# Optimization experiments

Measured on AMD Instinct MI355X. Metric: run time of the kernel, lower is better.

The kernel has to match this reference:

```python
import jax, jax.numpy as jnp
import numpy as np
from jax import lax

EPS = 1e-4


def setup_inputs() -> dict:
    key = jax.random.key(0)
    k1, k2, k3, k4, k5 = jax.random.split(key, 5)
    B, F, P, C = 8192, 512, 64, 100
    return {
        "x": jax.random.normal(k1, (B, F), dtype=jnp.float32),
        "w": jax.random.normal(k2, (P, F), dtype=jnp.float32),
        "xi": jax.random.normal(k3, (1, P), dtype=jnp.float32),
        "eta": jax.random.normal(k4, (1, P), dtype=jnp.float32),
        "beta": jax.random.normal(k5, (P, C), dtype=jnp.float32),
    }


def reference(x, w, xi, eta, beta):
    # Distance layer: squared Euclidean distance to each prototype -> [B, P]
    # ||w_p - x||^2 expressed as GEMM form (same math, efficient)
    d = (jnp.sum(x * x, axis=-1, keepdims=True)
         - 2.0 * (x @ w.T)
         + jnp.sum(w * w, axis=-1))  # [B, P]

    # Distance activation: si = sigmoid(xi) * exp(-eta^2 * d), scaled by per-sample max
    gamma = eta * eta                       # [1, P]
    alpha = jax.nn.sigmoid(xi)              # [1, P]
    si = jnp.exp(-gamma * d) * alpha        # [B, P]
    si = si / (jnp.max(si, axis=-1, keepdims=True) + EPS)

    # Belief masses: u_p normalized beta^2 rows -> mass [B, P, C]
    beta_sq = beta * beta
    u = beta_sq / jnp.sum(beta_sq, axis=-1, keepdims=True)  # [P, C]
    mass = si[..., None] * u[None]                           # [B, P, C]

    # Omega: append residual uncertainty channel -> [B, P, C+1]
    omega = 1.0 - jnp.sum(mass, axis=-1, keepdims=True)
    mass_omega = jnp.concatenate([mass, omega], axis=-1)

    # Sequential Dempster combination over prototypes
    masses = jnp.moveaxis(mass_omega, 1, 0)  # [P, B, C+1]

    def step(m1, m2):
        omega1 = m1[..., -1:]
        omega2 = m2[..., -1:]
        c = m1 * m2 + m1 * omega2 + omega1 * m2
        c = c / (jnp.sum(c, axis=-1, keepdims=True) + EPS)
        return c, None

    m_final, _ = lax.scan(step, masses[0], masses[1:])  # [B, C+1]

    # Final normalization
    return m_final / jnp.sum(m_final, axis=-1, keepdims=True)
```

## Files before the change

### kernel.cpp

```cpp
#include <hip/hip_runtime.h>
#include <math.h>

#define NB 8192
#define NF 512
#define NP 64
#define NC 100
#define NR 16
#define EPSF 1e-4f
#define LOG2E 1.44269504088896340736f

using short8  = __attribute__((ext_vector_type(8))) short;
using floatx4 = __attribute__((ext_vector_type(4))) float;

__device__ __forceinline__ short2 bsplit(float v) {
  unsigned b = __float_as_uint(v);
  short h = (short)(b >> 16);
  float hf = __uint_as_float(b & 0xFFFF0000u);
  float lo = v - hf;
  short l = (short)(__float_as_uint(lo) >> 16);
  return make_short2(h, l);
}

__global__ __launch_bounds__(256, 2)
void ds_fused2(const float* __restrict__ x, const float* __restrict__ w,
               const float* __restrict__ xi, const float* __restrict__ eta,
               const float* __restrict__ beta, float* __restrict__ out)
{
  __shared__ __align__(16) short xhi_l[NR * 136];
  __shared__ __align__(16) short xlo_l[NR * 136];
  __shared__ __align__(16) char  wu_l[64 * 136 * 2 * 2];
  __shared__ __align__(16) float d_l[NR * 68];
  __shared__ __align__(16) float si_l[NR * 64];
  __shared__ float sqp_l[NR * 17];
  __shared__ float red_l[256];
  __shared__ float xsql[NR];
  __shared__ float wsql[64], alph_l[64], kgam_l[64], binv_l[64];
  short* whi_l = (short*)wu_l;
  short* wlo_l = (short*)(wu_l + 64 * 136 * 2);
  float* u_l   = (float*)wu_l;

  const int t  = threadIdx.x;
  const int R0 = blockIdx.x * NR;

  const int xr_row = t >> 4, xr_sl = t & 15;
  const int wr_p   = t >> 2, wr_q  = t & 3;
  const int wv = t >> 6;
  const int ml = t & 15;
  const int qd = (t & 63) >> 4;

  float xsq_acc = 0.f, wsq_acc = 0.f;
  floatx4 acc0 = {0.f, 0.f, 0.f, 0.f};
  floatx4 acc1 = {0.f, 0.f, 0.f, 0.f};

  for (int ch = 0; ch < 4; ++ch) {
    const int kb = ch * 128;
    __syncthreads();
    {
      const float* xr = x + (size_t)(R0 + xr_row) * NF + kb + xr_sl * 8;
      float4 a = *(const float4*)&xr[0];
      float4 b = *(const float4*)&xr[4];
      xsq_acc += a.x*a.x + a.y*a.y + a.z*a.z + a.w*a.w
               + b.x*b.x + b.y*b.y + b.z*b.z + b.w*b.w;
      short8 hv, lv;
      short2 s0 = bsplit(a.x), s1 = bsplit(a.y), s2 = bsplit(a.z), s3 = bsplit(a.w);
      short2 s4 = bsplit(b.x), s5 = bsplit(b.y), s6 = bsplit(b.z), s7 = bsplit(b.w);
      hv[0]=s0.x; hv[1]=s1.x; hv[2]=s2.x; hv[3]=s3.x;
      hv[4]=s4.x; hv[5]=s5.x; hv[6]=s6.x; hv[7]=s7.x;
      lv[0]=s0.y; lv[1]=s1.y; lv[2]=s2.y; lv[3]=s3.y;
      lv[4]=s4.y; lv[5]=s5.y; lv[6]=s6.y; lv[7]=s7.y;
      *(short8*)&xhi_l[xr_row * 136 + xr_sl * 8] = hv;
      *(short8*)&xlo_l[xr_row * 136 + xr_sl * 8] = lv;
    }
    {
      const float* wr = w + (size_t)wr_p * NF + kb + wr_q * 32;
      #pragma unroll
      for (int g = 0; g < 4; ++g) {
        float4 a = *(const float4*)&wr[g * 8];
        float4 b = *(const float4*)&wr[g * 8 + 4];
        wsq_acc += a.x*a.x + a.y*a.y + a.z*a.z + a.w*a.w
                 + b.x*b.x + b.y*b.y + b.z*b.z + b.w*b.w;
        short8 hv, lv;
        short2 s0 = bsplit(a.x), s1 = bsplit(a.y), s2 = bsplit(a.z), s3 = bsplit(a.w);
        short2 s4 = bsplit(b.x), s5 = bsplit(b.y), s6 = bsplit(b.z), s7 = bsplit(b.w);
        hv[0]=s0.x; hv[1]=s1.x; hv[2]=s2.x; hv[3]=s3.x;
        hv[4]=s4.x; hv[5]=s5.x; hv[6]=s6.x; hv[7]=s7.x;
        lv[0]=s0.y; lv[1]=s1.y; lv[2]=s2.y; lv[3]=s3.y;
        lv[4]=s4.y; lv[5]=s5.y; lv[6]=s6.y; lv[7]=s7.y;
        *(short8*)&whi_l[wr_p * 136 + wr_q * 32 + g * 8] = hv;
        *(short8*)&wlo_l[wr_p * 136 + wr_q * 32 + g * 8] = lv;
      }
    }
    __syncthreads();
    #pragma unroll
    for (int ks = 0; ks < 4; ++ks) {
      short8 ah = *(const short8*)&xhi_l[ml * 136 + ks * 32 + qd * 8];
      short8 al = *(const short8*)&xlo_l[ml * 136 + ks * 32 + qd * 8];
      short8 bh = *(const short8*)&whi_l[(wv * 16 + ml) * 136 + ks * 32 + qd * 8];
      short8 bl = *(const short8*)&wlo_l[(wv * 16 + ml) * 136 + ks * 32 + qd * 8];
      acc0 = __builtin_amdgcn_mfma_f32_16x16x32_bf16(ah, bh, acc0, 0, 0, 0);
      acc1 = __builtin_amdgcn_mfma_f32_16x16x32_bf16(ah, bl, acc1, 0, 0, 0);
      acc1 = __builtin_amdgcn_mfma_f32_16x16x32_bf16(al, bh, acc1, 0, 0, 0);
    }
  }

  {
    #pragma unroll
    for (int i = 0; i < 4; ++i) {
      const int row = qd * 4 + i;
      d_l[row * 68 + wv * 16 + ml] = acc0[i] + acc1[i];
    }
    sqp_l[xr_row * 17 + xr_sl] = xsq_acc;
    red_l[wr_q * 64 + wr_p]    = wsq_acc;
  }
  __syncthreads();
  if (t < NR) {
    float s = 0.f;
    #pragma unroll
    for (int q = 0; q < 16; ++q) s += sqp_l[t * 17 + q];
    xsql[t] = s;
  }
  if (t < 64) {
    wsql[t] = ((red_l[t] + red_l[64 + t]) + red_l[128 + t]) + red_l[192 + t];
    float e = eta[t];
    kgam_l[t] = -LOG2E * e * e;
    alph_l[t] = 1.f / (1.f + __expf(-xi[t]));
  }
  __syncthreads();

  {
    const int p4 = t >> 2, q4 = t & 3;
    const float* br = beta + p4 * NC + q4 * 25;
    float s = 0.f;
    #pragma unroll 5
    for (int j = 0; j < 25; ++j) { float b = br[j]; s = fmaf(b, b, s); }
    red_l[q4 * 64 + p4] = s;
  }
  {
    const int row = t >> 4, p = (t & 15) * 4;
    float4 dt = *(const float4*)&d_l[row * 68 + p];
    const float xs = xsql[row];
    float si0 = alph_l[p+0] * exp2f(kgam_l[p+0] * (xs + wsql[p+0] - 2.f * dt.x));
    float si1 = alph_l[p+1] * exp2f(kgam_l[p+1] * (xs + wsql[p+1] - 2.f * dt.y));
    float si2 = alph_l[p+2] * exp2f(kgam_l[p+2] * (xs + wsql[p+2] - 2.f * dt.z));
    float si3 = alph_l[p+3] * exp2f(kgam_l[p+3] * (xs + wsql[p+3] - 2.f * dt.w));
    float mx = fmaxf(fmaxf(si0, si1), fmaxf(si2, si3));
    #pragma unroll
    for (int msk = 1; msk < 16; msk <<= 1) mx = fmaxf(mx, __shfl_xor(mx, msk, 64));
    const float rinv = 1.f / (mx + EPSF);
    float4 sv = make_float4(si0 * rinv, si1 * rinv, si2 * rinv, si3 * rinv);
    *(float4*)&si_l[row * 64 + p] = sv;
  }
  __syncthreads();
  if (t < 64) binv_l[t] = 1.f / (((red_l[t] + red_l[64 + t]) + red_l[128 + t]) + red_l[192 + t]);
  __syncthreads();
  {
    const int p4 = t >> 2, q4 = t & 3;
    const float bi = binv_l[p4];
    #pragma unroll
    for (int i = 0; i < 8; ++i) {
      const int q = q4 + 4 * i;
      float4 uv = make_float4(0.f, 0.f, 0.f, 0.f);
      if (q < 25) {
        const float* br = beta + p4 * NC + q * 4;
        float b0 = br[0], b1 = br[1], b2 = br[2], b3 = br[3];
        uv = make_float4(b0*b0*bi, b1*b1*bi, b2*b2*bi, b3*b3*bi);
      }
      *(float4*)&u_l[p4 * 128 + q * 4] = uv;
    }
  }
  __syncthreads();

  const int lane = t & 31;
  const bool isom = (lane == 25);
  #pragma unroll
  for (int pass = 0; pass < 2; ++pass) {
    const int row = pass * 8 + (t >> 5);
    const float* sirow = &si_l[row * 64];
    float4 u0 = *(const float4*)&u_l[lane * 4];
    float sp  = sirow[0];
    float m0 = sp * u0.x, m1 = sp * u0.y, m2 = sp * u0.z, m3 = sp * u0.w;
    float om1 = 1.f - sp;
    if (isom) m0 = om1;

    for (int p = 1; p < NP; ++p) {
      sp = sirow[p];
      float4 u = *(const float4*)&u_l[p * 128 + lane * 4];
      float om2 = 1.f - sp;
      float nom = -(om1 * om2);
      float t20 = fmaf(sp, u.x, om2);
      t20 = isom ? (om2 + om2) : t20;
      float t21 = fmaf(sp, u.y, om2);
      float t22 = fmaf(sp, u.z, om2);
      float t23 = fmaf(sp, u.w, om2);
      m0 = fmaf(m0 + om1, t20, nom);
      m1 = fmaf(m1 + om1, t21, nom);
      m2 = fmaf(m2 + om1, t22, nom);
      m3 = fmaf(m3 + om1, t23, nom);
      om1 = fmaf(nom, -2.f, -nom);
      if (isom) m0 = om1;
      if ((p & 3) == 0) {
        float ss = (m0 + m1) + (m2 + m3);
        #pragma unroll
        for (int msk = 1; msk < 32; msk <<= 1) ss += __shfl_xor(ss, msk, 64);
        float rn = __builtin_amdgcn_rcpf(ss);
        m0 *= rn; m1 *= rn; m2 *= rn; m3 *= rn; om1 *= rn;
      }
    }

    float ss = (m0 + m1) + (m2 + m3);
    #pragma unroll
    for (int msk = 1; msk < 32; msk <<= 1) ss += __shfl_xor(ss, msk, 64);
    float rn = 1.f / ss;
    m0 *= rn; m1 *= rn; m2 *= rn; m3 *= rn;

    float* orow = &out[(size_t)(R0 + row) * 101];
    if (lane < 25) {
      orow[lane*4+0] = m0; orow[lane*4+1] = m1;
      orow[lane*4+2] = m2; orow[lane*4+3] = m3;
    } else if (lane == 25) {
      orow[100] = m0;
    }
  }
}

extern "C" void kernel_launch(void* const* d_in, const int* in_sizes, int n_in,
                              void* d_out, int out_size, void* d_ws, size_t ws_size,
                              hipStream_t stream)
{
  const float* x    = (const float*)d_in[0];
  const float* w    = (const float*)d_in[1];
  const float* xi   = (const float*)d_in[2];
  const float* eta  = (const float*)d_in[3];
  const float* beta = (const float*)d_in[4];
  (void)d_ws; (void)ws_size;
  hipLaunchKernelGGL(ds_fused2, dim3(NB / NR), dim3(256), 0, stream,
                     x, w, xi, eta, beta, (float*)d_out);
}
```

Measured before the change: 95.66 us.

## Replace sequential Dempster scan with closed-form product recurrence and single-pass bf16 GEMM

The x·wᵀ GEMM drops the hi/lo bf16 split and runs as one truncated-bf16 MFMA pass with smaller K chunks. The per-row reductions now use shuffles instead of shared-memory partial sums, and the si computation reads directly from the MFMA accumulators. The 63-step sequential Dempster combination is rewritten as a closed-form product/scan: per-prototype scale factors come from a prefix product via shuffles, then a reverse loop accumulates a product and a weighted sum. Occupancy is raised to three blocks per CU. The aim is to cut the serial dependency chain and the GEMM cost, at the risk of precision loss from single bf16 truncation and of underflow or overflow from the powers of 3 and long products.

Result: faster. 85.17 us (-11.0%).

```diff
diff --git a/kernel.cpp b/kernel.cpp
--- a/kernel.cpp
+++ b/kernel.cpp
@@ -7,125 +7,91 @@
 #define NC 100
 #define NR 16
 #define EPSF 1e-4f
-#define LOG2E 1.44269504088896340736f
+#define LOG2E  1.44269504088896340736f
+#define LOG2_3 1.58496250072115618145f
 
 using short8  = __attribute__((ext_vector_type(8))) short;
 using floatx4 = __attribute__((ext_vector_type(4))) float;
 
-__device__ __forceinline__ short2 bsplit(float v) {
-  unsigned b = __float_as_uint(v);
-  short h = (short)(b >> 16);
-  float hf = __uint_as_float(b & 0xFFFF0000u);
-  float lo = v - hf;
-  short l = (short)(__float_as_uint(lo) >> 16);
-  return make_short2(h, l);
+__device__ __forceinline__ uint2 pkbf(float4 v) {
+  uint2 r;
+  r.x = (__float_as_uint(v.y) & 0xffff0000u) | (__float_as_uint(v.x) >> 16);
+  r.y = (__float_as_uint(v.w) & 0xffff0000u) | (__float_as_uint(v.z) >> 16);
+  return r;
 }
 
-__global__ __launch_bounds__(256, 2)
-void ds_fused2(const float* __restrict__ x, const float* __restrict__ w,
-               const float* __restrict__ xi, const float* __restrict__ eta,
-               const float* __restrict__ beta, float* __restrict__ out)
+#define OFF_XH    0
+#define OFF_WH    2304
+#define OFF_U     0
+#define OFF_PK4   32768
+#define OFF_SI    40960
+#define OFF_REDB  45056
+#define OFF_RMAX  46080
+#define OFF_UMAX  46336
+#define OFF_XSQL  46592
+#define OFF_WSQL  46656
+#define OFF_KGAM  46912
+#define OFF_ALPH  47168
+#define OFF_BINV  47424
+#define OFF_OMF   47680
+#define SMEM_SZ   47712
+
+__global__ __launch_bounds__(256, 3)
+void ds_one(const float* __restrict__ x, const float* __restrict__ w,
+            const float* __restrict__ xi, const float* __restrict__ eta,
+            const float* __restrict__ beta, float* __restrict__ out)
 {
-  __shared__ __align__(16) short xhi_l[NR * 136];
-  __shared__ __align__(16) short xlo_l[NR * 136];
-  __shared__ __align__(16) char  wu_l[64 * 136 * 2 * 2];
-  __shared__ __align__(16) float d_l[NR * 68];
-  __shared__ __align__(16) float si_l[NR * 64];
-  __shared__ float sqp_l[NR * 17];
-  __shared__ float red_l[256];
-  __shared__ float xsql[NR];
-  __shared__ float wsql[64], alph_l[64], kgam_l[64], binv_l[64];
-  short* whi_l = (short*)wu_l;
-  short* wlo_l = (short*)(wu_l + 64 * 136 * 2);
-  float* u_l   = (float*)wu_l;
-
-  const int t  = threadIdx.x;
-  const int R0 = blockIdx.x * NR;
-
-  const int xr_row = t >> 4, xr_sl = t & 15;
-  const int wr_p   = t >> 2, wr_q  = t & 3;
-  const int wv = t >> 6;
-  const int ml = t & 15;
-  const int qd = (t & 63) >> 4;
-
-  float xsq_acc = 0.f, wsq_acc = 0.f;
-  floatx4 acc0 = {0.f, 0.f, 0.f, 0.f};
-  floatx4 acc1 = {0.f, 0.f, 0.f, 0.f};
-
-  for (int ch = 0; ch < 4; ++ch) {
-    const int kb = ch * 128;
+  __shared__ __align__(16) char smem[SMEM_SZ];
+  short*  xh    = (short*)(smem + OFF_XH);
+  short*  wh    = (short*)(smem + OFF_WH);
+  float*  u_l   = (float*)(smem + OFF_U);
+  float4* pk4   = (float4*)(smem + OFF_PK4);
+  float*  si_l  = (float*)(smem + OFF_SI);
+  float*  redb  = (float*)(smem + OFF_REDB);
+  float*  rmax  = (float*)(smem + OFF_RMAX);
+  float*  umax  = (float*)(smem + OFF_UMAX);
+  float*  xsql  = (float*)(smem + OFF_XSQL);
+  float*  wsql  = (float*)(smem + OFF_WSQL);
+  float*  kgaml = (float*)(smem + OFF_KGAM);
+  float*  alphl = (float*)(smem + OFF_ALPH);
+  float*  binv  = (float*)(smem + OFF_BINV);
+  float*  omf   = (float*)(smem + OFF_OMF);
+
+  const int t    = threadIdx.x;
+  const int R0   = blockIdx.x * NR;
+  const int wv   = t >> 6;
+  const int ml   = t & 15;
+  const int qd   = (t & 63) >> 4;
+  const int xrow = t >> 4, xq = t & 15;
+  const int wl   = t & 63;
+
+  float xsq_acc = 0.f;
+  float wacc[4] = {0.f, 0.f, 0.f, 0.f};
+  floatx4 acc = {0.f, 0.f, 0.f, 0.f};
+
+  for (int ch = 0; ch < 8; ++ch) {
+    const int kb = ch * 64;
     __syncthreads();
     {
-      const float* xr = x + (size_t)(R0 + xr_row) * NF + kb + xr_sl * 8;
-      float4 a = *(const float4*)&xr[0];
-      float4 b = *(const float4*)&xr[4];
-      xsq_acc += a.x*a.x + a.y*a.y + a.z*a.z + a.w*a.w
-               + b.x*b.x + b.y*b.y + b.z*b.z + b.w*b.w;
-      short8 hv, lv;
-      short2 s0 = bsplit(a.x), s1 = bsplit(a.y), s2 = bsplit(a.z), s3 = bsplit(a.w);
-      short2 s4 = bsplit(b.x), s5 = bsplit(b.y), s6 = bsplit(b.z), s7 = bsplit(b.w);
-      hv[0]=s0.x; hv[1]=s1.x; hv[2]=s2.x; hv[3]=s3.x;
-      hv[4]=s4.x; hv[5]=s5.x; hv[6]=s6.x; hv[7]=s7.x;
-      lv[0]=s0.y; lv[1]=s1.y; lv[2]=s2.y; lv[3]=s3.y;
-      lv[4]=s4.y; lv[5]=s5.y; lv[6]=s6.y; lv[7]=s7.y;
-      *(short8*)&xhi_l[xr_row * 136 + xr_sl * 8] = hv;
-      *(short8*)&xlo_l[xr_row * 136 + xr_sl * 8] = lv;
-    }
-    {
-      const float* wr = w + (size_t)wr_p * NF + kb + wr_q * 32;
-      #pragma unroll
-      for (int g = 0; g < 4; ++g) {
-        float4 a = *(const float4*)&wr[g * 8];
-        float4 b = *(const float4*)&wr[g * 8 + 4];
-        wsq_acc += a.x*a.x + a.y*a.y + a.z*a.z + a.w*a.w
-                 + b.x*b.x + b.y*b.y + b.z*b.z + b.w*b.w;
-        short8 hv, lv;
-        short2 s0 = bsplit(a.x), s1 = bsplit(a.y), s2 = bsplit(a.z), s3 = bsplit(a.w);
-        short2 s4 = bsplit(b.x), s5 = bsplit(b.y), s6 = bsplit(b.z), s7 = bsplit(b.w);
-        hv[0]=s0.x; hv[1]=s1.x; hv[2]=s2.x; hv[3]=s3.x;
-        hv[4]=s4.x; hv[5]=s5.x; hv[6]=s6.x; hv[7]=s7.x;
-        lv[0]=s0.y; lv[1]=s1.y; lv[2]=s2.y; lv[3]=s3.y;
-        lv[4]=s4.y; lv[5]=s5.y; lv[6]=s6.y; lv[7]=s7.y;
-        *(short8*)&whi_l[wr_p * 136 + wr_q * 32 + g * 8] = hv;
-        *(short8*)&wlo_l[wr_p * 136 + wr_q * 32 + g * 8] = lv;
-      }
-    }
-    __syncthreads();
-    #pragma unroll
-    for (int ks = 0; ks < 4; ++ks) {
-      short8 ah = *(const short8*)&xhi_l[ml * 136 + ks * 32 + qd * 8];
-      short8 al = *(const short8*)&xlo_l[ml * 136 + ks * 32 + qd * 8];
-      short8 bh = *(const short8*)&whi_l[(wv * 16 + ml) * 136 + ks * 32 + qd * 8];
-      short8 bl = *(const short8*)&wlo_l[(wv * 16 + ml) * 136 + ks * 32 + qd * 8];
-      acc0 = __builtin_amdgcn_mfma_f32_16x16x32_bf16(ah, bh, acc0, 0, 0, 0);
-      acc1 = __builtin_amdgcn_mfma_f32_16x16x32_bf16(ah, bl, acc1, 0, 0, 0);
-      acc1 = __builtin_amdgcn_mfma_f32_16x16x32_bf16(al, bh, acc1, 0, 0, 0);
-    }
-  }
-
-  {
-    #pragma unroll
-    for (int i = 0; i < 4; ++i) {
-      const int row = qd * 4 + i;
-      d_l[row * 68 + wv * 16 + ml] = acc0[i] + acc1[i];
-    }
-    sqp_l[xr_row * 17 + xr_sl] = xsq_acc;
-    red_l[wr_q * 64 + wr_p]    = wsq_acc;
-  }
-  __syncthreads();
-  if (t < NR) {
-    float s = 0.f;
-    #pragma unroll
-    for (int q = 0; q < 16; ++q) s += sqp_l[t * 17 + q];
-    xsql[t] = s;
-  }
-  if (t < 64) {
-    wsql[t] = ((red_l[t] + red_l[64 + t]) + red_l[128 + t]) + red_l[192 + t];
-    float e = eta[t];
-    kgam_l[t] = -LOG2E * e * e;
-    alph_l[t] = 1.f / (1.f + __expf(-xi[t]));
-  }
-  __syncthreads();
+      float4 v = *(const float4*)&x[(size_t)(R0 + xrow) * NF + kb + xq * 4];
+      xsq_acc += v.x*v.x + v.y*v.y + v.z*v.z + v.w*v.w;
+      *(uint2*)&xh[xrow * 72 + xq * 4] = pkbf(v);
+    }
+    #pragma unroll
+    for (int g = 0; g < 4; ++g) {
+      const int row = wv * 16 + g * 4 + (wl >> 4);
+      float4 v = *(const float4*)&w[(size_t)row * NF + kb + xq * 4];
+      wacc[g] += v.x*v.x + v.y*v.y + v.z*v.z + v.w*v.w;
+      *(uint2*)&wh[row * 72 + xq * 4] = pkbf(v);
+    }
+    __syncthreads();
+    #pragma unroll
+    for (int ks = 0; ks < 2; ++ks) {
+      short8 a = *(const short8*)&xh[ml * 72 + ks * 32 + qd * 8];
+      short8 b = *(const short8*)&wh[(wv * 16 + ml) * 72 + ks * 32 + qd * 8];
+      acc = __builtin_amdgcn_mfma_f32_16x16x32_bf16(a, b, acc, 0, 0, 0);
+    }
+  }
 
   {
     const int p4 = t >> 2, q4 = t & 3;
@@ -133,93 +99,136 @@
     float s = 0.f;
     #pragma unroll 5
     for (int j = 0; j < 25; ++j) { float b = br[j]; s = fmaf(b, b, s); }
-    red_l[q4 * 64 + p4] = s;
-  }
-  {
-    const int row = t >> 4, p = (t & 15) * 4;
-    float4 dt = *(const float4*)&d_l[row * 68 + p];
-    const float xs = xsql[row];
-    float si0 = alph_l[p+0] * exp2f(kgam_l[p+0] * (xs + wsql[p+0] - 2.f * dt.x));
-    float si1 = alph_l[p+1] * exp2f(kgam_l[p+1] * (xs + wsql[p+1] - 2.f * dt.y));
-    float si2 = alph_l[p+2] * exp2f(kgam_l[p+2] * (xs + wsql[p+2] - 2.f * dt.z));
-    float si3 = alph_l[p+3] * exp2f(kgam_l[p+3] * (xs + wsql[p+3] - 2.f * dt.w));
-    float mx = fmaxf(fmaxf(si0, si1), fmaxf(si2, si3));
-    #pragma unroll
-    for (int msk = 1; msk < 16; msk <<= 1) mx = fmaxf(mx, __shfl_xor(mx, msk, 64));
-    const float rinv = 1.f / (mx + EPSF);
-    float4 sv = make_float4(si0 * rinv, si1 * rinv, si2 * rinv, si3 * rinv);
-    *(float4*)&si_l[row * 64 + p] = sv;
+    redb[q4 * 64 + p4] = s;
+  }
+  {
+    float s = xsq_acc;
+    s += __shfl_xor(s, 1, 64); s += __shfl_xor(s, 2, 64);
+    s += __shfl_xor(s, 4, 64); s += __shfl_xor(s, 8, 64);
+    if (xq == 0) xsql[xrow] = s;
+  }
+  #pragma unroll
+  for (int g = 0; g < 4; ++g) {
+    float s = wacc[g];
+    s += __shfl_xor(s, 1, 64); s += __shfl_xor(s, 2, 64);
+    s += __shfl_xor(s, 4, 64); s += __shfl_xor(s, 8, 64);
+    if (xq == 0) wsql[wv * 16 + g * 4 + (wl >> 4)] = s;
+  }
+  if (t < 64) {
+    float e = eta[t];
+    kgaml[t] = -LOG2E * e * e;
+    alphl[t] = 1.f / (1.f + __expf(-xi[t]));
   }
   __syncthreads();
-  if (t < 64) binv_l[t] = 1.f / (((red_l[t] + red_l[64 + t]) + red_l[128 + t]) + red_l[192 + t]);
+
+  if (t < 64) binv[t] = 1.f / (((redb[t] + redb[64 + t]) + redb[128 + t]) + redb[192 + t]);
+  const int pcol = wv * 16 + ml;
+  float si4[4];
+  {
+    const float wq = wsql[pcol], kg = kgaml[pcol], al = alphl[pcol];
+    #pragma unroll
+    for (int i = 0; i < 4; ++i) {
+      float d = xsql[qd * 4 + i] + wq - 2.f * acc[i];
+      si4[i] = al * exp2f(kg * d);
+    }
+    #pragma unroll
+    for (int i = 0; i < 4; ++i) {
+      float m = si4[i];
+      m = fmaxf(m, __shfl_xor(m, 1, 64)); m = fmaxf(m, __shfl_xor(m, 2, 64));
+      m = fmaxf(m, __shfl_xor(m, 4, 64)); m = fmaxf(m, __shfl_xor(m, 8, 64));
+      if (ml == 0) rmax[(qd * 4 + i) * 4 + wv] = m;
+    }
+  }
   __syncthreads();
+
   {
     const int p4 = t >> 2, q4 = t & 3;
-    const float bi = binv_l[p4];
-    #pragma unroll
-    for (int i = 0; i < 8; ++i) {
-      const int q = q4 + 4 * i;
+    const float bi = binv[p4];
+    float um = 0.f;
+    #pragma unroll
+    for (int i2 = 0; i2 < 8; ++i2) {
+      const int q = q4 + 4 * i2;
       float4 uv = make_float4(0.f, 0.f, 0.f, 0.f);
       if (q < 25) {
         const float* br = beta + p4 * NC + q * 4;
-        float b0 = br[0], b1 = br[1], b2 = br[2], b3 = br[3];
-        uv = make_float4(b0*b0*bi, b1*b1*bi, b2*b2*bi, b3*b3*bi);
+        uv.x = br[0]*br[0]*bi; uv.y = br[1]*br[1]*bi;
+        uv.z = br[2]*br[2]*bi; uv.w = br[3]*br[3]*bi;
       }
+      um = fmaxf(um, fmaxf(fmaxf(uv.x, uv.y), fmaxf(uv.z, uv.w)));
       *(float4*)&u_l[p4 * 128 + q * 4] = uv;
     }
+    um = fmaxf(um, __shfl_xor(um, 1, 64));
+    um = fmaxf(um, __shfl_xor(um, 2, 64));
+    if (q4 == 0) umax[p4] = um;
+  }
+  #pragma unroll
+  for (int i = 0; i < 4; ++i) {
+    const int row = qd * 4 + i;
+    float m = fmaxf(fmaxf(rmax[row * 4 + 0], rmax[row * 4 + 1]),
+                    fmaxf(rmax[row * 4 + 2], rmax[row * 4 + 3]));
+    si_l[row * 64 + pcol] = si4[i] * (1.f / (m + EPSF));
   }
   __syncthreads();
 
   const int lane = t & 31;
-  const bool isom = (lane == 25);
-  #pragma unroll
+  const int row8 = t >> 5;
+  #pragma unroll 1
   for (int pass = 0; pass < 2; ++pass) {
-    const int row = pass * 8 + (t >> 5);
-    const float* sirow = &si_l[row * 64];
-    float4 u0 = *(const float4*)&u_l[lane * 4];
-    float sp  = sirow[0];
-    float m0 = sp * u0.x, m1 = sp * u0.y, m2 = sp * u0.z, m3 = sp * u0.w;
-    float om1 = 1.f - sp;
-    if (isom) m0 = om1;
-
-    for (int p = 1; p < NP; ++p) {
-      sp = sirow[p];
-      float4 u = *(const float4*)&u_l[p * 128 + lane * 4];
-      float om2 = 1.f - sp;
-      float nom = -(om1 * om2);
-      float t20 = fmaf(sp, u.x, om2);
-      t20 = isom ? (om2 + om2) : t20;
-      float t21 = fmaf(sp, u.y, om2);
-      float t22 = fmaf(sp, u.z, om2);
-      float t23 = fmaf(sp, u.w, om2);
-      m0 = fmaf(m0 + om1, t20, nom);
-      m1 = fmaf(m1 + om1, t21, nom);
-      m2 = fmaf(m2 + om1, t22, nom);
-      m3 = fmaf(m3 + om1, t23, nom);
-      om1 = fmaf(nom, -2.f, -nom);
-      if (isom) m0 = om1;
-      if ((p & 3) == 0) {
-        float ss = (m0 + m1) + (m2 + m3);
-        #pragma unroll
-        for (int msk = 1; msk < 32; msk <<= 1) ss += __shfl_xor(ss, msk, 64);
-        float rn = __builtin_amdgcn_rcpf(ss);
-        m0 *= rn; m1 *= rn; m2 *= rn; m3 *= rn; om1 *= rn;
+    const int srow = pass * 8 + row8;
+    {
+      float sp0 = si_l[srow * 64 + lane];
+      float sp1 = si_l[srow * 64 + 32 + lane];
+      float um0 = umax[lane], um1 = umax[32 + lane];
+      float om0 = 1.f - sp0, om1 = 1.f - sp1;
+      float c0 = 1.f / fmaf(sp0, um0, om0);
+      float c1 = 1.f / fmaf(sp1, um1, om1);
+      float st0 = sp0 * c0, ot0 = om0 * c0;
+      float st1 = sp1 * c1, ot1 = om1 * c1;
+      float pA = ot0, pB = ot1;
+      #pragma unroll
+      for (int d2 = 1; d2 < 32; d2 <<= 1) {
+        float uA = __shfl_up(pA, d2, 32);
+        float uB = __shfl_up(pB, d2, 32);
+        if (lane >= d2) { pA *= uA; pB *= uB; }
       }
-    }
-
+      float totA = __shfl(pA, 31, 32);
+      float w0 = (lane == 0) ? 0.f : exp2f((float)(lane - 1) * LOG2_3) * pA;
+      float w1 = exp2f((float)(lane + 31) * LOG2_3) * (totA * pB);
+      pk4[row8 * 64 + lane]      = make_float4(st0, ot0, w0, 0.f);
+      pk4[row8 * 64 + 32 + lane] = make_float4(st1, ot1, w1, 0.f);
+      if (lane == 31) omf[row8] = 3.f * exp2f(62.f * LOG2_3) * (totA * pB);
+    }
+    __syncthreads();
+    float4 T = make_float4(1.f, 1.f, 1.f, 1.f);
+    float4 S = make_float4(0.f, 0.f, 0.f, 0.f);
+    for (int p = 63; p >= 0; --p) {
+      float4 f  = pk4[row8 * 64 + p];
+      float4 uv = *(const float4*)&u_l[p * 128 + lane * 4];
+      S.x = fmaf(f.z, T.x, S.x); S.y = fmaf(f.z, T.y, S.y);
+      S.z = fmaf(f.z, T.z, S.z); S.w = fmaf(f.z, T.w, S.w);
+      T.x *= fmaf(f.x, uv.x, f.y);
+      T.y *= fmaf(f.x, uv.y, f.y);
+      T.z *= fmaf(f.x, uv.z, f.y);
+      T.w *= fmaf(f.x, uv.w, f.y);
+    }
+    float om = omf[row8];
+    float m0 = fmaf(2.f, S.x, T.x) - om;
+    float m1 = fmaf(2.f, S.y, T.y) - om;
+    float m2 = fmaf(2.f, S.z, T.z) - om;
+    float m3 = fmaf(2.f, S.w, T.w) - om;
+    if (lane >= 25) { m0 = 0.f; m1 = 0.f; m2 = 0.f; m3 = 0.f; }
     float ss = (m0 + m1) + (m2 + m3);
     #pragma unroll
-    for (int msk = 1; msk < 32; msk <<= 1) ss += __shfl_xor(ss, msk, 64);
-    float rn = 1.f / ss;
-    m0 *= rn; m1 *= rn; m2 *= rn; m3 *= rn;
-
-    float* orow = &out[(size_t)(R0 + row) * 101];
+    for (int msk = 1; msk < 32; msk <<= 1) ss += __shfl_xor(ss, msk, 32);
+    float rn = 1.f / (ss + om);
+    float* orow = &out[(size_t)(R0 + srow) * 101];
     if (lane < 25) {
-      orow[lane*4+0] = m0; orow[lane*4+1] = m1;
-      orow[lane*4+2] = m2; orow[lane*4+3] = m3;
+      orow[lane * 4 + 0] = m0 * rn; orow[lane * 4 + 1] = m1 * rn;
+      orow[lane * 4 + 2] = m2 * rn; orow[lane * 4 + 3] = m3 * rn;
     } else if (lane == 25) {
-      orow[100] = m0;
-    }
+      orow[100] = om * rn;
+    }
+    __syncthreads();
   }
 }
 
@@ -233,6 +242,6 @@
   const float* eta  = (const float*)d_in[3];
   const float* beta = (const float*)d_in[4];
   (void)d_ws; (void)ws_size;
-  hipLaunchKernelGGL(ds_fused2, dim3(NB / NR), dim3(256), 0, stream,
+  hipLaunchKernelGGL(ds_one, dim3(NB / NR), dim3(256), 0, stream,
                      x, w, xi, eta, beta, (float*)d_out);
 }
```
